# Performance work log

Measured on AMD Instinct MI355X. Metric: run time of the kernel, lower is better.

Reference implementation:

```python
import jax, jax.numpy as jnp
from jax import lax
import numpy as np


def setup_inputs() -> dict:
    key = jax.random.key(0)
    k1, k2, k3 = jax.random.split(key, 3)
    B, X, Y, Z = 8, 128, 128, 128
    P = 64  # total persons across the batch
    feature = jax.random.normal(k1, (B, X, Y, Z), dtype=jnp.float32)
    # float batch indices in [0, B)
    batch_index = jnp.floor(jax.random.uniform(k2, (P,), dtype=jnp.float32) * B)
    # positions inside the voxel grid extent
    person_pos = jax.random.uniform(k3, (P, 3), dtype=jnp.float32) * jnp.array([X - 1, Y - 1, Z - 1], jnp.float32)
    min_loc_xyz = jnp.zeros((3,), jnp.float32)
    loc_delta_xyz = jnp.ones((3,), jnp.float32)
    return {"feature": feature, "batch_index": batch_index, "person_pos": person_pos,
            "min_loc_xyz": min_loc_xyz, "loc_delta_xyz": loc_delta_xyz}


def reference(feature, batch_index, person_pos, min_loc_xyz, loc_delta_xyz):
    B, X, Y, Z = feature.shape
    max_idx = jnp.array([X - 1, Y - 1, Z - 1], jnp.float32)
    # PersonPosToIndexes: world coords -> clipped voxel indices (round via +0.5 cast)
    idx = jnp.clip((person_pos - min_loc_xyz) / loc_delta_xyz, 0.0, max_idx)  # [P,3]
    full = jnp.concatenate([batch_index[:, None], idx], axis=-1)  # [P,4]
    ii = (full + 0.5).astype(jnp.int32)
    # PersonPosToHeatMap: sparse scatter of ones into dense volume
    heat = jnp.zeros(feature.shape, feature.dtype).at[ii[:, 0], ii[:, 1], ii[:, 2], ii[:, 3]].set(1.0)
    # HeatMapToWeights: 3x3x3 max-pool dilation (SAME, stride 1)
    dil = lax.reduce_window(heat, jnp.float32(-jnp.inf), lax.max,
                            (1, 3, 3, 3), (1, 1, 1, 1), 'SAME')
    nr_persons = jnp.sum(heat, axis=(1, 2, 3))  # [B]
    nr_positions = jnp.float32(X * Y * Z)
    scale_neg = (nr_persons * 27.0 / nr_positions)[:, None, None, None]
    scale_pos = (1.0 - nr_persons / nr_positions)[:, None, None, None]
    weights = (1.0 - dil) * scale_neg + heat * scale_pos
    # weighted MSE reduced per batch element, normalized by person count
    se = (feature - heat) ** 2
    loss = jnp.sum(se * weights, axis=(1, 2, 3)) / nr_persons
    return loss
```

## Files before the change

kernel.cpp:

```cpp
#include <hip/hip_runtime.h>

#define BATCH     8
#define DIM       128
#define NVOX      (BATCH * DIM * DIM * DIM)
#define NPERSON   64
#define THREADS   256
#define FLOATS_PER_BLOCK 8192
#define NBLOCK1   (NVOX / FLOATS_PER_BLOCK)
#define TSIZE     4096
#define EMPTYK    0xFFFFFFFFu

__global__ __launch_bounds__(THREADS) void sumsq_kernel(
    const float* __restrict__ feature, float* __restrict__ partials)
{
    const int tid = threadIdx.x;
    const float4* f4 = (const float4*)feature;
    const size_t base = (size_t)blockIdx.x * (FLOATS_PER_BLOCK / 4);
    float acc = 0.f;
#pragma unroll
    for (int j = 0; j < 8; ++j) {
        float4 v = f4[base + (size_t)j * THREADS + tid];
        acc += v.x * v.x + v.y * v.y + v.z * v.z + v.w * v.w;
    }
    for (int off = 32; off > 0; off >>= 1) acc += __shfl_down(acc, off, 64);
    __shared__ float wsum[4];
    const int lane = tid & 63, wave = tid >> 6;
    if (lane == 0) wsum[wave] = acc;
    __syncthreads();
    if (tid == 0) partials[blockIdx.x] = wsum[0] + wsum[1] + wsum[2] + wsum[3];
}

__global__ __launch_bounds__(THREADS) void finalize_kernel(
    const float* __restrict__ feature,
    const float* __restrict__ batch_index,
    const float* __restrict__ person_pos,
    const float* __restrict__ min_loc,
    const float* __restrict__ delta,
    const float* __restrict__ partials,
    float* __restrict__ out)
{
    __shared__ unsigned keys[NPERSON];
    __shared__ int      uniq[NPERSON];
    __shared__ float    sS2[BATCH], sDil[BATCH], sCorr[BATCH], sPos[BATCH];
    __shared__ int      sNr[BATCH];
    __shared__ unsigned table[TSIZE];
    __shared__ float    red[4];

    const int tid = threadIdx.x;

    if (tid < BATCH) { sDil[tid] = 0.f; sCorr[tid] = 0.f; sPos[tid] = 0.f; sNr[tid] = 0; }
    for (int s = tid; s < TSIZE; s += THREADS) table[s] = EMPTYK;

    if (tid < NPERSON) {
        const int p = tid;
        const int b = (int)(batch_index[p] + 0.5f);
        float vx = (person_pos[p * 3 + 0] - min_loc[0]) / delta[0];
        float vy = (person_pos[p * 3 + 1] - min_loc[1]) / delta[1];
        float vz = (person_pos[p * 3 + 2] - min_loc[2]) / delta[2];
        vx = fminf(fmaxf(vx, 0.f), (float)(DIM - 1));
        vy = fminf(fmaxf(vy, 0.f), (float)(DIM - 1));
        vz = fminf(fmaxf(vz, 0.f), (float)(DIM - 1));
        const int x = (int)(vx + 0.5f);
        const int y = (int)(vy + 0.5f);
        const int z = (int)(vz + 0.5f);
        keys[p] = ((unsigned)b << 21) | ((unsigned)x << 14) | ((unsigned)y << 7) | (unsigned)z;
    }
    __syncthreads();

    if (tid < NPERSON) {
        int u = 1;
        for (int q = 0; q < tid; ++q)
            if (keys[q] == keys[tid]) { u = 0; break; }
        uniq[tid] = u;
        if (u) atomicAdd(&sNr[keys[tid] >> 21], 1);
    }
    __syncthreads();

    for (int w = tid; w < NPERSON * 27; w += THREADS) {
        const int p = w / 27;
        if (!uniq[p]) continue;
        const unsigned k = keys[p];
        const int o = w % 27;
        const int x = (int)((k >> 14) & 127) + (o / 9) - 1;
        const int y = (int)((k >> 7) & 127) + ((o / 3) % 3) - 1;
        const int z = (int)(k & 127) + (o % 3) - 1;
        if ((unsigned)x > (unsigned)(DIM - 1) || (unsigned)y > (unsigned)(DIM - 1) ||
            (unsigned)z > (unsigned)(DIM - 1)) continue;
        const unsigned nk = (k & (7u << 21)) | ((unsigned)x << 14) | ((unsigned)y << 7) | (unsigned)z;
        unsigned h = ((nk * 2654435761u) >> 16) & (TSIZE - 1);
        for (;;) {
            const unsigned old = atomicCAS(&table[h], EMPTYK, nk);
            if (old == EMPTYK || old == nk) break;
            h = (h + 1) & (TSIZE - 1);
        }
    }
    __syncthreads();

    for (int s = tid; s < TSIZE; s += THREADS) {
        const unsigned k = table[s];
        if (k == EMPTYK) continue;
        const int b = k >> 21;
        const int x = (k >> 14) & 127, y = (k >> 7) & 127, z = k & 127;
        const float f = feature[(((size_t)b * DIM + x) * DIM + y) * DIM + z];
        float heat = 0.f;
        for (int q = 0; q < NPERSON; ++q)
            if (keys[q] == k) { heat = 1.f; break; }
        const float d = f - heat;
        atomicAdd(&sDil[b], d * d);
    }

    if (tid < NPERSON && uniq[tid]) {
        const unsigned k = keys[tid];
        const int b = k >> 21;
        const int x = (k >> 14) & 127, y = (k >> 7) & 127, z = k & 127;
        const float f = feature[(((size_t)b * DIM + x) * DIM + y) * DIM + z];
        atomicAdd(&sCorr[b], 1.f - 2.f * f);
        const float d = f - 1.f;
        atomicAdd(&sPos[b], d * d);
    }

    const int lane = tid & 63, wave = tid >> 6;
    for (int b = 0; b < BATCH; ++b) {
        float v = partials[b * (NBLOCK1 / BATCH) + tid];
        for (int off = 32; off > 0; off >>= 1) v += __shfl_down(v, off, 64);
        if (lane == 0) red[wave] = v;
        __syncthreads();
        if (tid == 0) sS2[b] = red[0] + red[1] + red[2] + red[3];
        __syncthreads();
    }

    if (tid < BATCH) {
        const int b = tid;
        const float nr = (float)sNr[b];
        const float N = (float)(DIM * DIM * DIM);
        const float scale_neg = nr * 27.f / N;
        const float scale_pos = 1.f - nr / N;
        const float neg = sS2[b] + sCorr[b] - sDil[b];
        out[b] = (scale_neg * neg + scale_pos * sPos[b]) / nr;
    }
}

extern "C" void kernel_launch(void* const* d_in, const int* in_sizes, int n_in,
                              void* d_out, int out_size, void* d_ws, size_t ws_size,
                              hipStream_t stream)
{
    const float* feature     = (const float*)d_in[0];
    const float* batch_index = (const float*)d_in[1];
    const float* person_pos  = (const float*)d_in[2];
    const float* min_loc     = (const float*)d_in[3];
    const float* delta       = (const float*)d_in[4];
    float* out = (float*)d_out;
    float* partials = (float*)d_ws;

    sumsq_kernel<<<NBLOCK1, THREADS, 0, stream>>>(feature, partials);
    finalize_kernel<<<1, THREADS, 0, stream>>>(feature, batch_index, person_pos,
                                               min_loc, delta, partials, out);
}
```

Before: 120.6 us.

## Fuse sum-of-squares and finalize into one kernel with last-block reduction

Merges the two launches into one grid, with an extra block that does the person/hash-table work at the same time as the streaming sum-of-squares blocks. The final reduction runs in whichever block arrives last at an atomic counter, after a threadfence. This removes one kernel launch and overlaps the serial single-block work with the bandwidth-bound pass. In exchange it adds a memset of the counter before each launch, and the fused block uses more shared memory, which could lower occupancy for the streaming blocks.

Measured after the change: 166.2 us. +37.8%, slower.

```diff
diff --git a/kernel.cpp b/kernel.cpp
--- a/kernel.cpp
+++ b/kernel.cpp
@@ -10,118 +10,143 @@
 #define TSIZE     4096
 #define EMPTYK    0xFFFFFFFFu
 
-__global__ __launch_bounds__(THREADS) void sumsq_kernel(
-    const float* __restrict__ feature, float* __restrict__ partials)
-{
-    const int tid = threadIdx.x;
-    const float4* f4 = (const float4*)feature;
-    const size_t base = (size_t)blockIdx.x * (FLOATS_PER_BLOCK / 4);
-    float acc = 0.f;
-#pragma unroll
-    for (int j = 0; j < 8; ++j) {
-        float4 v = f4[base + (size_t)j * THREADS + tid];
-        acc += v.x * v.x + v.y * v.y + v.z * v.z + v.w * v.w;
-    }
-    for (int off = 32; off > 0; off >>= 1) acc += __shfl_down(acc, off, 64);
-    __shared__ float wsum[4];
-    const int lane = tid & 63, wave = tid >> 6;
-    if (lane == 0) wsum[wave] = acc;
-    __syncthreads();
-    if (tid == 0) partials[blockIdx.x] = wsum[0] + wsum[1] + wsum[2] + wsum[3];
-}
+#define WS_DIL   2048
+#define WS_CORR  2056
+#define WS_POS   2064
+#define WS_NR    2072
+#define WS_CNT   2080
 
-__global__ __launch_bounds__(THREADS) void finalize_kernel(
+__global__ __launch_bounds__(THREADS) void person_loss_fused(
     const float* __restrict__ feature,
     const float* __restrict__ batch_index,
     const float* __restrict__ person_pos,
     const float* __restrict__ min_loc,
     const float* __restrict__ delta,
-    const float* __restrict__ partials,
+    float* __restrict__ ws,
     float* __restrict__ out)
 {
     __shared__ unsigned keys[NPERSON];
     __shared__ int      uniq[NPERSON];
-    __shared__ float    sS2[BATCH], sDil[BATCH], sCorr[BATCH], sPos[BATCH];
-    __shared__ int      sNr[BATCH];
+    __shared__ float    lDil[BATCH], lCorr[BATCH], lPos[BATCH];
+    __shared__ int      lNr[BATCH];
     __shared__ unsigned table[TSIZE];
     __shared__ float    red[4];
+    __shared__ float    sS2[BATCH];
+    __shared__ int      isFinal;
 
-    const int tid = threadIdx.x;
+    const int tid  = threadIdx.x;
+    const int bid  = blockIdx.x;
+    const int lane = tid & 63, wave = tid >> 6;
+    unsigned* counter = (unsigned*)(ws + WS_CNT);
 
-    if (tid < BATCH) { sDil[tid] = 0.f; sCorr[tid] = 0.f; sPos[tid] = 0.f; sNr[tid] = 0; }
-    for (int s = tid; s < TSIZE; s += THREADS) table[s] = EMPTYK;
+    if (bid < NBLOCK1) {
+        const float4* f4 = (const float4*)feature;
+        const size_t base = (size_t)bid * (FLOATS_PER_BLOCK / 4);
+        float acc = 0.f;
+#pragma unroll
+        for (int j = 0; j < 8; ++j) {
+            float4 v = f4[base + (size_t)j * THREADS + tid];
+            acc += v.x * v.x + v.y * v.y + v.z * v.z + v.w * v.w;
+        }
+        for (int off = 32; off > 0; off >>= 1) acc += __shfl_down(acc, off, 64);
+        if (lane == 0) red[wave] = acc;
+        __syncthreads();
+        if (tid == 0) ws[bid] = red[0] + red[1] + red[2] + red[3];
+    } else {
+        if (tid < BATCH) { lDil[tid] = 0.f; lCorr[tid] = 0.f; lPos[tid] = 0.f; lNr[tid] = 0; }
+        for (int s = tid; s < TSIZE; s += THREADS) table[s] = EMPTYK;
 
-    if (tid < NPERSON) {
-        const int p = tid;
-        const int b = (int)(batch_index[p] + 0.5f);
-        float vx = (person_pos[p * 3 + 0] - min_loc[0]) / delta[0];
-        float vy = (person_pos[p * 3 + 1] - min_loc[1]) / delta[1];
-        float vz = (person_pos[p * 3 + 2] - min_loc[2]) / delta[2];
-        vx = fminf(fmaxf(vx, 0.f), (float)(DIM - 1));
-        vy = fminf(fmaxf(vy, 0.f), (float)(DIM - 1));
-        vz = fminf(fmaxf(vz, 0.f), (float)(DIM - 1));
-        const int x = (int)(vx + 0.5f);
-        const int y = (int)(vy + 0.5f);
-        const int z = (int)(vz + 0.5f);
-        keys[p] = ((unsigned)b << 21) | ((unsigned)x << 14) | ((unsigned)y << 7) | (unsigned)z;
+        if (tid < NPERSON) {
+            const int p = tid;
+            const int b = (int)(batch_index[p] + 0.5f);
+            float vx = (person_pos[p * 3 + 0] - min_loc[0]) / delta[0];
+            float vy = (person_pos[p * 3 + 1] - min_loc[1]) / delta[1];
+            float vz = (person_pos[p * 3 + 2] - min_loc[2]) / delta[2];
+            vx = fminf(fmaxf(vx, 0.f), (float)(DIM - 1));
+            vy = fminf(fmaxf(vy, 0.f), (float)(DIM - 1));
+            vz = fminf(fmaxf(vz, 0.f), (float)(DIM - 1));
+            const int x = (int)(vx + 0.5f);
+            const int y = (int)(vy + 0.5f);
+            const int z = (int)(vz + 0.5f);
+            keys[p] = ((unsigned)b << 21) | ((unsigned)x << 14) | ((unsigned)y << 7) | (unsigned)z;
+        }
+        __syncthreads();
+
+        if (tid < NPERSON) {
+            int u = 1;
+            for (int q = 0; q < tid; ++q)
+                if (keys[q] == keys[tid]) { u = 0; break; }
+            uniq[tid] = u;
+            if (u) atomicAdd(&lNr[keys[tid] >> 21], 1);
+        }
+        __syncthreads();
+
+        for (int w = tid; w < NPERSON * 27; w += THREADS) {
+            const int p = w / 27;
+            if (!uniq[p]) continue;
+            const unsigned k = keys[p];
+            const int o = w % 27;
+            const int x = (int)((k >> 14) & 127) + (o / 9) - 1;
+            const int y = (int)((k >> 7) & 127) + ((o / 3) % 3) - 1;
+            const int z = (int)(k & 127) + (o % 3) - 1;
+            if ((unsigned)x > (unsigned)(DIM - 1) || (unsigned)y > (unsigned)(DIM - 1) ||
+                (unsigned)z > (unsigned)(DIM - 1)) continue;
+            const unsigned nk = (k & (7u << 21)) | ((unsigned)x << 14) | ((unsigned)y << 7) | (unsigned)z;
+            unsigned h = ((nk * 2654435761u) >> 16) & (TSIZE - 1);
+            for (;;) {
+                const unsigned old = atomicCAS(&table[h], EMPTYK, nk);
+                if (old == EMPTYK || old == nk) break;
+                h = (h + 1) & (TSIZE - 1);
+            }
+        }
+        __syncthreads();
+
+        for (int s = tid; s < TSIZE; s += THREADS) {
+            const unsigned k = table[s];
+            if (k == EMPTYK) continue;
+            const int b = k >> 21;
+            const int x = (k >> 14) & 127, y = (k >> 7) & 127, z = k & 127;
+            const float f = feature[(((size_t)b * DIM + x) * DIM + y) * DIM + z];
+            float heat = 0.f;
+            for (int q = 0; q < NPERSON; ++q)
+                if (keys[q] == k) { heat = 1.f; break; }
+            const float d = f - heat;
+            atomicAdd(&lDil[b], d * d);
+        }
+
+        if (tid < NPERSON && uniq[tid]) {
+            const unsigned k = keys[tid];
+            const int b = k >> 21;
+            const int x = (k >> 14) & 127, y = (k >> 7) & 127, z = k & 127;
+            const float f = feature[(((size_t)b * DIM + x) * DIM + y) * DIM + z];
+            atomicAdd(&lCorr[b], 1.f - 2.f * f);
+            const float d = f - 1.f;
+            atomicAdd(&lPos[b], d * d);
+        }
+        __syncthreads();
+
+        if (tid == 0) {
+#pragma unroll
+            for (int b = 0; b < BATCH; ++b) {
+                ws[WS_DIL  + b] = lDil[b];
+                ws[WS_CORR + b] = lCorr[b];
+                ws[WS_POS  + b] = lPos[b];
+                ws[WS_NR   + b] = (float)lNr[b];
+            }
+        }
+    }
+
+    if (tid == 0) {
+        __threadfence();
+        const unsigned old = atomicAdd(counter, 1u);
+        isFinal = (old == (unsigned)NBLOCK1);
     }
     __syncthreads();
+    if (!isFinal) return;
 
-    if (tid < NPERSON) {
-        int u = 1;
-        for (int q = 0; q < tid; ++q)
-            if (keys[q] == keys[tid]) { u = 0; break; }
-        uniq[tid] = u;
-        if (u) atomicAdd(&sNr[keys[tid] >> 21], 1);
-    }
-    __syncthreads();
-
-    for (int w = tid; w < NPERSON * 27; w += THREADS) {
-        const int p = w / 27;
-        if (!uniq[p]) continue;
-        const unsigned k = keys[p];
-        const int o = w % 27;
-        const int x = (int)((k >> 14) & 127) + (o / 9) - 1;
-        const int y = (int)((k >> 7) & 127) + ((o / 3) % 3) - 1;
-        const int z = (int)(k & 127) + (o % 3) - 1;
-        if ((unsigned)x > (unsigned)(DIM - 1) || (unsigned)y > (unsigned)(DIM - 1) ||
-            (unsigned)z > (unsigned)(DIM - 1)) continue;
-        const unsigned nk = (k & (7u << 21)) | ((unsigned)x << 14) | ((unsigned)y << 7) | (unsigned)z;
-        unsigned h = ((nk * 2654435761u) >> 16) & (TSIZE - 1);
-        for (;;) {
-            const unsigned old = atomicCAS(&table[h], EMPTYK, nk);
-            if (old == EMPTYK || old == nk) break;
-            h = (h + 1) & (TSIZE - 1);
-        }
-    }
-    __syncthreads();
-
-    for (int s = tid; s < TSIZE; s += THREADS) {
-        const unsigned k = table[s];
-        if (k == EMPTYK) continue;
-        const int b = k >> 21;
-        const int x = (k >> 14) & 127, y = (k >> 7) & 127, z = k & 127;
-        const float f = feature[(((size_t)b * DIM + x) * DIM + y) * DIM + z];
-        float heat = 0.f;
-        for (int q = 0; q < NPERSON; ++q)
-            if (keys[q] == k) { heat = 1.f; break; }
-        const float d = f - heat;
-        atomicAdd(&sDil[b], d * d);
-    }
-
-    if (tid < NPERSON && uniq[tid]) {
-        const unsigned k = keys[tid];
-        const int b = k >> 21;
-        const int x = (k >> 14) & 127, y = (k >> 7) & 127, z = k & 127;
-        const float f = feature[(((size_t)b * DIM + x) * DIM + y) * DIM + z];
-        atomicAdd(&sCorr[b], 1.f - 2.f * f);
-        const float d = f - 1.f;
-        atomicAdd(&sPos[b], d * d);
-    }
-
-    const int lane = tid & 63, wave = tid >> 6;
+    __threadfence();
     for (int b = 0; b < BATCH; ++b) {
-        float v = partials[b * (NBLOCK1 / BATCH) + tid];
+        float v = ws[b * (NBLOCK1 / BATCH) + tid];
         for (int off = 32; off > 0; off >>= 1) v += __shfl_down(v, off, 64);
         if (lane == 0) red[wave] = v;
         __syncthreads();
@@ -131,12 +156,12 @@
 
     if (tid < BATCH) {
         const int b = tid;
-        const float nr = (float)sNr[b];
+        const float nr = ws[WS_NR + b];
         const float N = (float)(DIM * DIM * DIM);
         const float scale_neg = nr * 27.f / N;
         const float scale_pos = 1.f - nr / N;
-        const float neg = sS2[b] + sCorr[b] - sDil[b];
-        out[b] = (scale_neg * neg + scale_pos * sPos[b]) / nr;
+        const float neg = sS2[b] + ws[WS_CORR + b] - ws[WS_DIL + b];
+        out[b] = (scale_neg * neg + scale_pos * ws[WS_POS + b]) / nr;
     }
 }
 
@@ -150,9 +175,10 @@
     const float* min_loc     = (const float*)d_in[3];
     const float* delta       = (const float*)d_in[4];
     float* out = (float*)d_out;
-    float* partials = (float*)d_ws;
+    float* ws  = (float*)d_ws;
 
-    sumsq_kernel<<<NBLOCK1, THREADS, 0, stream>>>(feature, partials);
-    finalize_kernel<<<1, THREADS, 0, stream>>>(feature, batch_index, person_pos,
-                                               min_loc, delta, partials, out);
+    hipMemsetAsync((char*)d_ws + WS_CNT * sizeof(float), 0, sizeof(unsigned), stream);
+
+    person_loss_fused<<<NBLOCK1 + 1, THREADS, 0, stream>>>(
+        feature, batch_index, person_pos, min_loc, delta, ws, out);
 }
```
